# Kernel optimization log

Measured on AMD Instinct MI355X. Metric: run time of the kernel, lower is better.

## Reference

```python
import jax, jax.numpy as jnp
import numpy as np

HIDDEN = 1024
CUTOFFS = [20000, 80000, 200000]
PROJECT_FACTOR = 4
NUM_TAILS = len(CUTOFFS) - 1
CUTOFF_ENDS = [0] + CUTOFFS
BATCH, SEQ = 8, 1024


def _glorot(key, shape):
    fan_in, fan_out = shape
    limit = np.sqrt(6.0 / (fan_in + fan_out)).astype(np.float32)
    return jax.random.uniform(key, shape, jnp.float32, -limit, limit)


def setup_inputs() -> dict:
    key = jax.random.key(0)
    ks = jax.random.split(key, 7)
    return {
        "x": jax.random.randint(ks[0], (BATCH, SEQ), 0, CUTOFFS[-1], dtype=jnp.int64.dtype if jax.config.jax_enable_x64 else jnp.int32),
        "head_weight_proj": _glorot(ks[1], (HIDDEN, HIDDEN)),
        "head_weight": _glorot(ks[2], (HIDDEN, CUTOFFS[0] + NUM_TAILS)),
        "tail_weight_proj_0": _glorot(ks[3], (HIDDEN, HIDDEN // PROJECT_FACTOR)),
        "tail_weight_0": _glorot(ks[4], (HIDDEN // PROJECT_FACTOR, CUTOFFS[1] - CUTOFFS[0])),
        "tail_weight_proj_1": _glorot(ks[5], (HIDDEN, HIDDEN // PROJECT_FACTOR ** 2)),
        "tail_weight_1": _glorot(ks[6], (HIDDEN // PROJECT_FACTOR ** 2, CUTOFFS[2] - CUTOFFS[1])),
    }


def reference(x, head_weight_proj, head_weight, tail_weight_proj_0,
              tail_weight_0, tail_weight_proj_1, tail_weight_1) -> jnp.ndarray:
    # Faithful to AdaptiveEmbedding.compute_embeddings:
    #   tables[i] = weight.T (head truncated to cutoffs[0] rows), projs[i] = proj.T
    #   per-cluster: gather rows of table for in-range ids, matmul with proj,
    #   scatter back into y; here expressed densely with masks (same math,
    #   fixed shapes; out-of-cluster tokens contribute exactly zero).
    tables = [head_weight.T[:CUTOFFS[0]], tail_weight_0.T, tail_weight_1.T]
    projs = [head_weight_proj.T, tail_weight_proj_0.T, tail_weight_proj_1.T]
    y = jnp.zeros(x.shape + (HIDDEN,), dtype=jnp.float32)
    for i in range(len(CUTOFF_ENDS) - 1):
        l_idx, r_idx = CUTOFF_ENDS[i], CUTOFF_ENDS[i + 1]
        mask = (x >= l_idx) & (x < r_idx)                  # [B,S]
        idx = jnp.where(mask, x - l_idx, 0)                # in-range gather ids
        emb = tables[i][idx]                               # [B,S,d_i]
        proj = jnp.einsum('bsd,dh->bsh', emb, projs[i])    # [B,S,H]
        y = y + jnp.where(mask[..., None], proj, 0.0)
    emb_scale = jnp.asarray(HIDDEN ** 0.5, y.dtype)
    return y * emb_scale
```

## Files before the change

kernel.cpp:

```cpp
#include <hip/hip_runtime.h>
#include <hip/hip_bf16.h>

#define NTOK 8192
#define HID 1024
#define C0_END 20000
#define C1_END 80000
#define S0 20002
#define S1 60000
#define S2 120000

#define CAP0 1280
#define CAP1 3072
#define CAP2 6144
#define TS0 (CAP0/32)
#define TS1 (CAP1/32)
#define TS2 (CAP2/32)

#define NBUCK 12500

#define NW0 79
#define NW1 235
#define NW2 469

#define OFF_CNT 0
#define OFF_SST 16
#define OFF_BB  32
#define OFF_LS  50048
#define OFF_LI  (OFF_LS + NTOK*3*4)
#define OFF_W0  (OFF_LI + NTOK*3*4)
#define OFF_W1  (OFF_W0 + 1024*1024*2)
#define OFF_W2  (OFF_W1 + 256*1024*2)
#define OFF_A0  (OFF_W2 + 64*1024*2)
#define OFF_A1  (OFF_A0 + CAP0*1024*2)
#define OFF_A2  (OFF_A1 + CAP1*256*2)

typedef __attribute__((ext_vector_type(8))) short bf16x8;
typedef __attribute__((ext_vector_type(4))) float f32x4;

__device__ __forceinline__ unsigned short f2bf(float f) {
    union { __hip_bfloat16 b; unsigned short u; } cv;
    cv.b = __float2bfloat16(f);
    return cv.u;
}


__global__ void k_init(unsigned* __restrict__ bb, int* __restrict__ cnt) {
    int gid = blockIdx.x * 256 + threadIdx.x, stride = gridDim.x * 256;
    for (int i = gid; i < NBUCK; i += stride) bb[i] = 0u;
    if (gid < 3) cnt[gid] = 0;
}

__global__ void k_count(const int* __restrict__ x, int* __restrict__ cnt,
                        unsigned* __restrict__ bb) {
    int s = blockIdx.x * 256 + threadIdx.x;
    int lane = threadIdx.x & 63;
    int v = x[s];
    atomicAdd(&bb[v >> 4], 1u);
    int c = (v < C0_END) ? 0 : (v < C1_END ? 1 : 2);
    unsigned long long m0 = __ballot(c == 0);
    unsigned long long m1 = __ballot(c == 1);
    unsigned long long m2 = __ballot(c == 2);
    unsigned long long mymask = (c == 0) ? m0 : (c == 1) ? m1 : m2;
    int leader = __builtin_ctzll(mymask);
    if (lane == leader) atomicAdd(&cnt[c], __popcll(mymask));
}

__global__ __launch_bounds__(1024) void k_scan(unsigned* __restrict__ bb,
                                               unsigned* __restrict__ sstart) {
    __shared__ unsigned psum[16];
    int t = threadIdx.x, lane = t & 63, w = t >> 6;
    int base = t * 13;
    unsigned loc[13];
    unsigned s = 0;
#pragma unroll
    for (int i = 0; i < 13; i++) {
        int idx = base + i;
        unsigned v = (idx < NBUCK) ? bb[idx] : 0u;
        loc[i] = v; s += v;
    }
    unsigned inc = s;
    for (int d = 1; d < 64; d <<= 1) {
        unsigned o = __shfl_up(inc, d);
        if (lane >= d) inc += o;
    }
    if (lane == 63) psum[w] = inc;
    __syncthreads();
    if (w == 0) {
        unsigned ws = (lane < 16) ? psum[lane] : 0u;
        for (int d = 1; d < 16; d <<= 1) {
            unsigned o = __shfl_up(ws, d);
            if (lane >= d) ws += o;
        }
        if (lane < 16) psum[lane] = ws;
    }
    __syncthreads();
    unsigned excl = inc - s + ((w > 0) ? psum[w - 1] : 0u);
#pragma unroll
    for (int i = 0; i < 13; i++) {
        int idx = base + i;
        if (idx < NBUCK) bb[idx] = excl;
        excl += loc[i];
    }
    __syncthreads();
    if (t == 0) { sstart[0] = 0u; sstart[1] = bb[1250]; sstart[2] = bb[5000]; }
}

__global__ void k_scatter(const int* __restrict__ x, unsigned* __restrict__ bb,
                          const unsigned* __restrict__ sstart,
                          int* __restrict__ ls, int* __restrict__ li) {
    int s = blockIdx.x * 256 + threadIdx.x;
    int v = x[s];
    int c    = (v < C0_END) ? 0 : (v < C1_END ? 1 : 2);
    int base = (c == 0) ? 0 : (c == 1) ? C0_END : C1_END;
    unsigned cap = (c == 0) ? CAP0 : (c == 1) ? CAP1 : CAP2;
    unsigned pos = atomicAdd(&bb[v >> 4], 1u) - sstart[c];
    if (pos < cap) {
        ls[c * NTOK + pos] = s;
        li[c * NTOK + pos] = v - base;
    }
}

template <int KS>
__device__ __forceinline__ size_t frag_base4(int m, int r) {
    return ((size_t)(((m >> 5) * KS + (r >> 5)) * 2 + ((m >> 4) & 1)) << 9)
         + (size_t)((((m & 15) + (((r >> 3) & 3) << 4)) << 3) + (r & 7));
}

template <int RQL2, int V, int S, int KS, int CAPC, int B0, int NBC>
__device__ __forceinline__ void extract_item(int itL, int lane,
                                             float* __restrict__ lbuf,
                                             const float* __restrict__ t,
                                             const unsigned* __restrict__ bbEnd,
                                             const int* __restrict__ li,
                                             unsigned sstc,
                                             unsigned short* __restrict__ A) {
    int w  = itL >> RQL2;
    int rq = itL & ((1 << RQL2) - 1);
    int r  = rq * 4;
    int colbase = w << 8;
    int b0 = B0 + w * 16;
    int blast = min(b0 + 15, B0 + NBC - 1);
    unsigned pst = (b0 == 0) ? 0u : bbEnd[b0 - 1];
    unsigned pen = bbEnd[blast];
    if (pen <= pst) return;
    int colc = min(colbase + lane * 4, V - 4);
    const float* rowp = t + (size_t)r * S + colc;
    float4 v0 = *(const float4*)(rowp);
    float4 v1 = *(const float4*)(rowp + S);
    float4 v2 = *(const float4*)(rowp + 2 * (size_t)S);
    float4 v3 = *(const float4*)(rowp + 3 * (size_t)S);
    *(float4*)(lbuf + 0 * 256 + lane * 4) = v0;
    *(float4*)(lbuf + 1 * 256 + lane * 4) = v1;
    *(float4*)(lbuf + 2 * 256 + lane * 4) = v2;
    *(float4*)(lbuf + 3 * 256 + lane * 4) = v3;
    unsigned nt = pen - pst;
    for (unsigned ch = 0; ch < nt; ch += 64) {
        int cnum = (int)min(64u, nt - ch);
        if (lane < cnum) {
            int m = (int)(pst + ch - sstc) + lane;
            if ((unsigned)m < (unsigned)CAPC) {
                int cc = li[m] - colbase;
                float f0 = lbuf[0 * 256 + cc];
                float f1 = lbuf[1 * 256 + cc];
                float f2 = lbuf[2 * 256 + cc];
                float f3 = lbuf[3 * 256 + cc];
                unsigned p0 = (unsigned)f2bf(f0) | ((unsigned)f2bf(f1) << 16);
                unsigned p1 = (unsigned)f2bf(f2) | ((unsigned)f2bf(f3) << 16);
                uint2 pk = { p0, p1 };
                *(uint2*)(A + frag_base4<KS>(m, r)) = pk;
            }
        }
    }
}

#define EX_I0 (NW0 << 8)
#define EX_I1 (NW1 << 6)
#define EX_I2 (NW2 << 4)

__global__ __launch_bounds__(256) void k_extract(
        const float* __restrict__ t0, const float* __restrict__ t1,
        const float* __restrict__ t2,
        const float* __restrict__ hwp, const float* __restrict__ twp0,
        const float* __restrict__ twp1,
        const unsigned* __restrict__ bb, const unsigned* __restrict__ sstart,
        const int* __restrict__ li,
        unsigned short* __restrict__ A0, unsigned short* __restrict__ A1,
        unsigned short* __restrict__ A2,
        unsigned short* __restrict__ W0, unsigned short* __restrict__ W1,
        unsigned short* __restrict__ W2) {
    __shared__ float smem[4][4 * 256];
    int gid = blockIdx.x * 256 + threadIdx.x, stride = gridDim.x * 256;
    for (int i = gid; i < (1024 * 1024) / 4; i += stride) {
        float4 v = ((const float4*)hwp)[i];
        ushort4 o = { f2bf(v.x), f2bf(v.y), f2bf(v.z), f2bf(v.w) };
        ((ushort4*)W0)[i] = o;
    }
    for (int i = gid; i < (1024 * 256) / 4; i += stride) {
        float4 v = ((const float4*)twp0)[i];
        ushort4 o = { f2bf(v.x), f2bf(v.y), f2bf(v.z), f2bf(v.w) };
        ((ushort4*)W1)[i] = o;
    }
    for (int i = gid; i < (1024 * 64) / 4; i += stride) {
        float4 v = ((const float4*)twp1)[i];
        ushort4 o = { f2bf(v.x), f2bf(v.y), f2bf(v.z), f2bf(v.w) };
        ((ushort4*)W2)[i] = o;
    }
    int lane = threadIdx.x & 63;
    float* lbuf = smem[threadIdx.x >> 6];
    unsigned sst1 = sstart[1], sst2 = sstart[2];
    int wid = blockIdx.x * (blockDim.x >> 6) + (threadIdx.x >> 6);
    int nw  = gridDim.x * (blockDim.x >> 6);
    const int tot = EX_I0 + EX_I1 + EX_I2;
    for (int it = wid; it < tot; it += nw) {
        if (it < EX_I0)
            extract_item<8, 20000, S0, 32, CAP0, 0, 1250>(
                it, lane, lbuf, t0, bb, li, 0u, A0);
        else if (it < EX_I0 + EX_I1)
            extract_item<6, 60000, S1, 8, CAP1, 1250, 3750>(
                it - EX_I0, lane, lbuf, t1, bb, li + NTOK, sst1, A1);
        else
            extract_item<4, 120000, S2, 2, CAP2, 5000, 7500>(
                it - EX_I0 - EX_I1, lane, lbuf, t2, bb, li + 2 * NTOK, sst2, A2);
    }
}

template <int K>
__device__ __forceinline__ void gemm_body(int tile, int n, int lane, int wave, int by,
                                          const unsigned short* __restrict__ Ap,
                                          const unsigned short* __restrict__ Wb,
                                          const int* __restrict__ ls,
                                          float* __restrict__ out) {
    constexpr int KS = K / 32;
    int m0 = tile * 32;
    int lr = lane & 15, lg = lane >> 4;
    int hb = by * 256 + wave * 64;
    const unsigned short* abase = Ap + (size_t)tile * KS * 1024 + lane * 8;
    const unsigned short* bbase = Wb + (size_t)(hb + lr) * K + lg * 8;
    f32x4 acc[2][4] = {};
#pragma unroll 4
    for (int ks = 0; ks < KS; ks++) {
        bf16x8 a0 = *(const bf16x8*)(abase + ks * 1024);
        bf16x8 a1 = *(const bf16x8*)(abase + ks * 1024 + 512);
        bf16x8 b0 = *(const bf16x8*)(bbase + ks * 32);
        bf16x8 b1 = *(const bf16x8*)(bbase + ks * 32 + 16 * K);
        bf16x8 b2 = *(const bf16x8*)(bbase + ks * 32 + 32 * K);
        bf16x8 b3 = *(const bf16x8*)(bbase + ks * 32 + 48 * K);
        acc[0][0] = __builtin_amdgcn_mfma_f32_16x16x32_bf16(a0, b0, acc[0][0], 0, 0, 0);
        acc[0][1] = __builtin_amdgcn_mfma_f32_16x16x32_bf16(a0, b1, acc[0][1], 0, 0, 0);
        acc[0][2] = __builtin_amdgcn_mfma_f32_16x16x32_bf16(a0, b2, acc[0][2], 0, 0, 0);
        acc[0][3] = __builtin_amdgcn_mfma_f32_16x16x32_bf16(a0, b3, acc[0][3], 0, 0, 0);
        acc[1][0] = __builtin_amdgcn_mfma_f32_16x16x32_bf16(a1, b0, acc[1][0], 0, 0, 0);
        acc[1][1] = __builtin_amdgcn_mfma_f32_16x16x32_bf16(a1, b1, acc[1][1], 0, 0, 0);
        acc[1][2] = __builtin_amdgcn_mfma_f32_16x16x32_bf16(a1, b2, acc[1][2], 0, 0, 0);
        acc[1][3] = __builtin_amdgcn_mfma_f32_16x16x32_bf16(a1, b3, acc[1][3], 0, 0, 0);
    }
#pragma unroll
    for (int mf = 0; mf < 2; mf++)
#pragma unroll
        for (int r = 0; r < 4; r++) {
            int m = mf * 16 + lg * 4 + r;
            if (m0 + m < n) {
                int s = ls[m0 + m];
                float* orow = out + (size_t)s * HID + hb + lr;
                orow[0]  = 32.f * acc[mf][0][r];
                orow[16] = 32.f * acc[mf][1][r];
                orow[32] = 32.f * acc[mf][2][r];
                orow[48] = 32.f * acc[mf][3][r];
            }
        }
}

__global__ __launch_bounds__(256) void k_gemm(const int* __restrict__ cnt,
                                              const int* __restrict__ ls,
                                              const unsigned short* __restrict__ A0,
                                              const unsigned short* __restrict__ A1,
                                              const unsigned short* __restrict__ A2,
                                              const unsigned short* __restrict__ W0,
                                              const unsigned short* __restrict__ W1,
                                              const unsigned short* __restrict__ W2,
                                              float* __restrict__ out) {
    int bx = blockIdx.x;
    int lane = threadIdx.x & 63, wave = threadIdx.x >> 6;
    if (bx < TS0) {
        int n = min(cnt[0], CAP0); if (bx * 32 >= n) return;
        gemm_body<1024>(bx, n, lane, wave, blockIdx.y, A0, W0, ls, out);
    } else if (bx < TS0 + TS1) {
        int t = bx - TS0;
        int n = min(cnt[1], CAP1); if (t * 32 >= n) return;
        gemm_body<256>(t, n, lane, wave, blockIdx.y, A1, W1, ls + NTOK, out);
    } else {
        int t = bx - TS0 - TS1;
        int n = min(cnt[2], CAP2); if (t * 32 >= n) return;
        gemm_body<64>(t, n, lane, wave, blockIdx.y, A2, W2, ls + 2 * NTOK, out);
    }
}

extern "C" void kernel_launch(void* const* d_in, const int* in_sizes, int n_in,
                              void* d_out, int out_size, void* d_ws, size_t ws_size,
                              hipStream_t stream) {
    const int*   x    = (const int*)d_in[0];
    const float* hwp  = (const float*)d_in[1];
    const float* hw   = (const float*)d_in[2];
    const float* twp0 = (const float*)d_in[3];
    const float* tw0  = (const float*)d_in[4];
    const float* twp1 = (const float*)d_in[5];
    const float* tw1  = (const float*)d_in[6];

    char* ws = (char*)d_ws;
    int* cnt          = (int*)(ws + OFF_CNT);
    unsigned* sstart  = (unsigned*)(ws + OFF_SST);
    unsigned* bb      = (unsigned*)(ws + OFF_BB);
    int* ls           = (int*)(ws + OFF_LS);
    int* li           = (int*)(ws + OFF_LI);
    unsigned short* W0 = (unsigned short*)(ws + OFF_W0);
    unsigned short* W1 = (unsigned short*)(ws + OFF_W1);
    unsigned short* W2 = (unsigned short*)(ws + OFF_W2);
    unsigned short* A0 = (unsigned short*)(ws + OFF_A0);
    unsigned short* A1 = (unsigned short*)(ws + OFF_A1);
    unsigned short* A2 = (unsigned short*)(ws + OFF_A2);
    float* out = (float*)d_out;

    k_init<<<64, 256, 0, stream>>>(bb, cnt);
    k_count<<<NTOK / 256, 256, 0, stream>>>(x, cnt, bb);
    k_scan<<<1, 1024, 0, stream>>>(bb, sstart);
    k_scatter<<<NTOK / 256, 256, 0, stream>>>(x, bb, sstart, ls, li);
    k_extract<<<2048, 256, 0, stream>>>(hw, tw0, tw1, hwp, twp0, twp1,
                                        bb, sstart, li, A0, A1, A2, W0, W1, W2);
    k_gemm<<<dim3(TS0 + TS1 + TS2, 4), 256, 0, stream>>>(
        cnt, ls, A0, A1, A2, W0, W1, W2, out);
}
```

Measured before the change: 83.23 us.

## Restructure extract into block-level 16-row tiles with register prefetch pipelining

Extraction changes from per-wave 4-row x 256-column items to per-block 16-row x 256-column tiles staged in padded LDS. Global loads for the next tile are issued into registers before the current tile is processed, so memory latency overlaps the scatter work. It also drops the early-exit skip for empty buckets, so every tile is now loaded even when no token falls in that column range. It adds two block barriers per tile.

```diff
diff --git a/kernel.cpp b/kernel.cpp
--- a/kernel.cpp
+++ b/kernel.cpp
@@ -21,6 +21,9 @@
 #define NW0 79
 #define NW1 235
 #define NW2 469
+#define EXT0 (NW0 * 64)
+#define EXT1 (NW1 * 16)
+#define EXT2 (NW2 * 4)
 
 #define OFF_CNT 0
 #define OFF_SST 16
@@ -126,56 +129,56 @@
          + (size_t)((((m & 15) + (((r >> 3) & 3) << 4)) << 3) + (r & 7));
 }
 
-template <int RQL2, int V, int S, int KS, int CAPC, int B0, int NBC>
-__device__ __forceinline__ void extract_item(int itL, int lane,
-                                             float* __restrict__ lbuf,
-                                             const float* __restrict__ t,
+#define PAD 260
+
+template <int V, int S, int NW>
+__device__ __forceinline__ void issue_loads(int itL, int row, int cg,
+                                            const float* __restrict__ t,
+                                            float4 R[4]) {
+    int g = itL / NW, w = itL - g * NW;
+    int colbase = w << 8;
+    const float* rp = t + (size_t)(g * 16 + row) * S;
+#pragma unroll
+    for (int uu = 0; uu < 4; uu++) {
+        int col = min(colbase + cg * 4 + uu * 64, V - 4);
+        R[uu] = *(const float4*)(rp + col);
+    }
+}
+
+template <int KS, int CAPC, int B0, int NBC, int NW>
+__device__ __forceinline__ void process_item(int itL, int tid,
+                                             const float* __restrict__ lds,
                                              const unsigned* __restrict__ bbEnd,
                                              const int* __restrict__ li,
                                              unsigned sstc,
                                              unsigned short* __restrict__ A) {
-    int w  = itL >> RQL2;
-    int rq = itL & ((1 << RQL2) - 1);
-    int r  = rq * 4;
+    int g = itL / NW, w = itL - g * NW;
     int colbase = w << 8;
     int b0 = B0 + w * 16;
     int blast = min(b0 + 15, B0 + NBC - 1);
     unsigned pst = (b0 == 0) ? 0u : bbEnd[b0 - 1];
     unsigned pen = bbEnd[blast];
-    if (pen <= pst) return;
-    int colc = min(colbase + lane * 4, V - 4);
-    const float* rowp = t + (size_t)r * S + colc;
-    float4 v0 = *(const float4*)(rowp);
-    float4 v1 = *(const float4*)(rowp + S);
-    float4 v2 = *(const float4*)(rowp + 2 * (size_t)S);
-    float4 v3 = *(const float4*)(rowp + 3 * (size_t)S);
-    *(float4*)(lbuf + 0 * 256 + lane * 4) = v0;
-    *(float4*)(lbuf + 1 * 256 + lane * 4) = v1;
-    *(float4*)(lbuf + 2 * 256 + lane * 4) = v2;
-    *(float4*)(lbuf + 3 * 256 + lane * 4) = v3;
     unsigned nt = pen - pst;
+    int rq = tid & 3;
     for (unsigned ch = 0; ch < nt; ch += 64) {
-        int cnum = (int)min(64u, nt - ch);
-        if (lane < cnum) {
-            int m = (int)(pst + ch - sstc) + lane;
+        unsigned tloc = ch + (unsigned)(tid >> 2);
+        if (tloc < nt) {
+            int m = (int)(pst + tloc) - (int)sstc;
             if ((unsigned)m < (unsigned)CAPC) {
                 int cc = li[m] - colbase;
-                float f0 = lbuf[0 * 256 + cc];
-                float f1 = lbuf[1 * 256 + cc];
-                float f2 = lbuf[2 * 256 + cc];
-                float f3 = lbuf[3 * 256 + cc];
+                const float* lp = lds + (rq * 4) * PAD + cc;
+                float f0 = lp[0];
+                float f1 = lp[PAD];
+                float f2 = lp[2 * PAD];
+                float f3 = lp[3 * PAD];
                 unsigned p0 = (unsigned)f2bf(f0) | ((unsigned)f2bf(f1) << 16);
                 unsigned p1 = (unsigned)f2bf(f2) | ((unsigned)f2bf(f3) << 16);
                 uint2 pk = { p0, p1 };
-                *(uint2*)(A + frag_base4<KS>(m, r)) = pk;
+                *(uint2*)(A + frag_base4<KS>(m, g * 16 + rq * 4)) = pk;
             }
         }
     }
 }
-
-#define EX_I0 (NW0 << 8)
-#define EX_I1 (NW1 << 6)
-#define EX_I2 (NW2 << 4)
 
 __global__ __launch_bounds__(256) void k_extract(
         const float* __restrict__ t0, const float* __restrict__ t1,
@@ -188,7 +191,7 @@
         unsigned short* __restrict__ A2,
         unsigned short* __restrict__ W0, unsigned short* __restrict__ W1,
         unsigned short* __restrict__ W2) {
-    __shared__ float smem[4][4 * 256];
+    __shared__ float smem[16 * PAD];
     int gid = blockIdx.x * 256 + threadIdx.x, stride = gridDim.x * 256;
     for (int i = gid; i < (1024 * 1024) / 4; i += stride) {
         float4 v = ((const float4*)hwp)[i];
@@ -205,22 +208,47 @@
         ushort4 o = { f2bf(v.x), f2bf(v.y), f2bf(v.z), f2bf(v.w) };
         ((ushort4*)W2)[i] = o;
     }
-    int lane = threadIdx.x & 63;
-    float* lbuf = smem[threadIdx.x >> 6];
+    int tid = threadIdx.x;
+    int row = tid >> 4, cg = tid & 15;
     unsigned sst1 = sstart[1], sst2 = sstart[2];
-    int wid = blockIdx.x * (blockDim.x >> 6) + (threadIdx.x >> 6);
-    int nw  = gridDim.x * (blockDim.x >> 6);
-    const int tot = EX_I0 + EX_I1 + EX_I2;
-    for (int it = wid; it < tot; it += nw) {
-        if (it < EX_I0)
-            extract_item<8, 20000, S0, 32, CAP0, 0, 1250>(
-                it, lane, lbuf, t0, bb, li, 0u, A0);
-        else if (it < EX_I0 + EX_I1)
-            extract_item<6, 60000, S1, 8, CAP1, 1250, 3750>(
-                it - EX_I0, lane, lbuf, t1, bb, li + NTOK, sst1, A1);
+    int nb = gridDim.x;
+    const int tot = EXT0 + EXT1 + EXT2;
+    const int* li1 = li + NTOK;
+    const int* li2 = li + 2 * NTOK;
+    float4 R[4];
+    int it = blockIdx.x;
+    if (it < EXT0)             issue_loads<20000, S0, NW0>(it, row, cg, t0, R);
+    else if (it < EXT0 + EXT1) issue_loads<60000, S1, NW1>(it - EXT0, row, cg, t1, R);
+    else                       issue_loads<120000, S2, NW2>(it - EXT0 - EXT1, row, cg, t2, R);
+    while (it < tot) {
+        int nxt = it + nb;
+        asm volatile("s_waitcnt lgkmcnt(0)" ::: "memory");
+        __builtin_amdgcn_s_barrier();
+        __builtin_amdgcn_sched_barrier(0);
+        asm volatile("s_waitcnt vmcnt(0)" ::: "memory");
+        __builtin_amdgcn_sched_barrier(0);
+        {
+            float* dp = smem + row * PAD + cg * 4;
+            *(float4*)(dp + 0)   = R[0];
+            *(float4*)(dp + 64)  = R[1];
+            *(float4*)(dp + 128) = R[2];
+            *(float4*)(dp + 192) = R[3];
+        }
+        if (nxt < tot) {
+            if (nxt < EXT0)             issue_loads<20000, S0, NW0>(nxt, row, cg, t0, R);
+            else if (nxt < EXT0 + EXT1) issue_loads<60000, S1, NW1>(nxt - EXT0, row, cg, t1, R);
+            else                        issue_loads<120000, S2, NW2>(nxt - EXT0 - EXT1, row, cg, t2, R);
+        }
+        asm volatile("s_waitcnt lgkmcnt(0)" ::: "memory");
+        __builtin_amdgcn_s_barrier();
+        __builtin_amdgcn_sched_barrier(0);
+        if (it < EXT0)
+            process_item<32, CAP0, 0, 1250, NW0>(it, tid, smem, bb, li, 0u, A0);
+        else if (it < EXT0 + EXT1)
+            process_item<8, CAP1, 1250, 3750, NW1>(it - EXT0, tid, smem, bb, li1, sst1, A1);
         else
-            extract_item<4, 120000, S2, 2, CAP2, 5000, 7500>(
-                it - EX_I0 - EX_I1, lane, lbuf, t2, bb, li + 2 * NTOK, sst2, A2);
+            process_item<2, CAP2, 5000, 7500, NW2>(it - EXT0 - EXT1, tid, smem, bb, li2, sst2, A2);
+        it = nxt;
     }
 }
 
```

Result: slower. 132.6 us (+59.3%).
